# Kernel optimization log

Measured on AMD Instinct MI355X. Metric: run time of the kernel, lower is better.

Reference implementation:

```python
import jax, jax.numpy as jnp
import numpy as np
import math

B, S, E, H = 4, 4096, 2048, 16
Dh = E // H  # 128


def setup_inputs() -> dict:
    key = jax.random.key(0)
    ks = jax.random.split(key, 8)
    s = 1.0 / math.sqrt(E)
    return {
        "x": jax.random.normal(ks[0], (B, S, E), dtype=jnp.float32),
        "Wz": jax.random.uniform(ks[1], (E, E), jnp.float32, -s, s),
        "bz": jax.random.uniform(ks[2], (E,), jnp.float32, -s, s),
        "Wx": jax.random.uniform(ks[3], (E, E), jnp.float32, -s, s),
        "bx": jax.random.uniform(ks[4], (E,), jnp.float32, -s, s),
        "phase": jax.random.normal(ks[5], (H, Dh), dtype=jnp.float32),
        "Wo": jax.random.uniform(ks[6], (E, E), jnp.float32, -s, s),
        "bo": jax.random.uniform(ks[7], (E,), jnp.float32, -s, s),
    }


def reference(x, Wz, bz, Wx, bx, phase, Wo, bo):
    # torch nn.Linear: y = x @ W.T + b  (W stored [out, in])
    z = x @ Wz.T + bz                     # [B,S,E]
    xs = x @ Wx.T + bx                    # [B,S,E]
    z_h = z.reshape(B, S, H, Dh)
    x_h = xs.reshape(B, S, H, Dh)
    # elementwise phase modulation of query heads
    mod = z_h * jnp.sin(phase)            # [B,S,H,Dh] * [H,Dh]
    # NOTE: heads are on axis -2 (no transpose to [B,H,S,Dh]),
    # so scores contract over Dh giving per-token HEAD-mixing: [B,S,H,H]
    scores = jnp.einsum('bshd,bsgd->bshg', mod, x_h) / math.sqrt(Dh)
    w = jax.nn.softmax(scores, axis=-1)   # softmax over head axis g
    att = jnp.einsum('bshg,bsgd->bshd', w, x_h)  # [B,S,H,Dh]
    att = att.reshape(B, S, E)
    return att @ Wo.T + bo
```

## Files before the change

### kernel.cpp

```cpp
#include <hip/hip_runtime.h>
#include <hip/hip_bf16.h>

#define TOK 16384
#define E 2048
#define DH 128

using bf16x8 = __attribute__((ext_vector_type(8))) __bf16;
using f32x4  = __attribute__((ext_vector_type(4))) float;
using u16x8  = __attribute__((ext_vector_type(8))) unsigned short;

static __device__ __forceinline__ unsigned short f2bf(float f) {
  union { float f; unsigned u; } x; x.f = f;
  unsigned r = x.u + 0x7fffu + ((x.u >> 16) & 1u);
  return (unsigned short)(r >> 16);
}

static __device__ __forceinline__ void gload_lds16(const unsigned short* g, unsigned short* l) {
  __builtin_amdgcn_global_load_lds(
      (const __attribute__((address_space(1))) void*)g,
      (__attribute__((address_space(3))) void*)l, 16, 0, 0);
}

static __device__ __forceinline__ void cvt8(const float* __restrict__ src,
                                            unsigned short* __restrict__ dst,
                                            float sc) {
  const float4* p = reinterpret_cast<const float4*>(src);
  float4 v0 = p[0], v1 = p[1];
  u16x8 o;
  o[0] = f2bf(v0.x * sc); o[1] = f2bf(v0.y * sc); o[2] = f2bf(v0.z * sc); o[3] = f2bf(v0.w * sc);
  o[4] = f2bf(v1.x * sc); o[5] = f2bf(v1.y * sc); o[6] = f2bf(v1.z * sc); o[7] = f2bf(v1.w * sc);
  *reinterpret_cast<u16x8*>(dst) = o;
}

__global__ __launch_bounds__(256) void prep_all(const float* __restrict__ x,
                                                const float* __restrict__ Wz,
                                                const float* __restrict__ Wx,
                                                const float* __restrict__ Wo,
                                                const float* __restrict__ bz,
                                                const float* __restrict__ bx,
                                                const float* __restrict__ phase,
                                                unsigned short* __restrict__ x_bf,
                                                unsigned short* __restrict__ wzx,
                                                unsigned short* __restrict__ wo_bf,
                                                float* __restrict__ bzx) {
  const int N0 = TOK * E / 8;
  const int N1 = E * E / 8;
  const int NB = (2 * E) / 8;
  const float rs = 0.08838834764831845f;
  const int total = N0 + 3 * N1 + NB;
  const int stride = gridDim.x * blockDim.x;
  for (int i = blockIdx.x * blockDim.x + threadIdx.x; i < total; i += stride) {
    if (i < N0) {
      cvt8(x + (size_t)i * 8, x_bf + (size_t)i * 8, 1.0f);
    } else if (i < N0 + N1) {
      const int j = i - N0;
      const float sc = sinf(phase[j >> 8]) * rs;
      cvt8(Wz + (size_t)j * 8, wzx + (size_t)j * 8, sc);
    } else if (i < N0 + 2 * N1) {
      const int j = i - N0 - N1;
      cvt8(Wx + (size_t)j * 8, wzx + (size_t)E * E + (size_t)j * 8, 1.0f);
    } else if (i < N0 + 3 * N1) {
      const int j = i - N0 - 2 * N1;
      cvt8(Wo + (size_t)j * 8, wo_bf + (size_t)j * 8, 1.0f);
    } else {
      const int j = i - N0 - 3 * N1;
#pragma unroll
      for (int k = 0; k < 8; ++k) {
        const int idx = j * 8 + k;
        bzx[idx] = (idx < E) ? bz[idx] * sinf(phase[idx]) * rs : bx[idx - E];
      }
    }
  }
}

#define MFMA16 __builtin_amdgcn_mfma_f32_16x16x32_bf16

static __device__ __forceinline__ bf16x8 ldf(const unsigned short* buf, int row, int slot) {
  return *reinterpret_cast<const bf16x8*>(buf + row * 64 + ((slot ^ (row & 7)) << 3));
}

static __device__ __forceinline__ void stage_half(const unsigned short* gbase, int ld,
                                                  unsigned short* dsthalf,
                                                  int r, int slot, int wave) {
#pragma unroll
  for (int c = 0; c < 2; ++c)
    gload_lds16(gbase + (size_t)(c * 64 + r) * ld + slot * 8,
                dsthalf + c * 4096 + wave * 512);
}

static __device__ __forceinline__ void quad(f32x4 (&acc)[8][4], const bf16x8 (&a)[4][2],
                                            const bf16x8 (&b)[2][2], int mh, int nh) {
#pragma unroll
  for (int mi = 0; mi < 4; ++mi)
#pragma unroll
    for (int ni = 0; ni < 2; ++ni)
#pragma unroll
      for (int kk = 0; kk < 2; ++kk)
        acc[mh * 4 + mi][nh * 2 + ni] =
            MFMA16(a[mi][kk], b[ni][kk], acc[mh * 4 + mi][nh * 2 + ni], 0, 0, 0);
}

#define PH_BAR()  __builtin_amdgcn_s_barrier()
#define VMCNT(n)  asm volatile("s_waitcnt vmcnt(" #n ")" ::: "memory")
#define PRIO1()   __builtin_amdgcn_s_setprio(1)
#define PRIO0()   __builtin_amdgcn_s_setprio(0)

#define LD_A(dst, buf, base)                                             \
  _Pragma("unroll")                                                      \
  for (int mi = 0; mi < 4; ++mi)                                         \
    _Pragma("unroll")                                                    \
    for (int kk = 0; kk < 2; ++kk)                                       \
      dst[mi][kk] = ldf(buf, (base) + mi * 16, kk * 4 + grp);

#define LD_B(dst, buf, base)                                             \
  _Pragma("unroll")                                                      \
  for (int ni = 0; ni < 2; ++ni)                                         \
    _Pragma("unroll")                                                    \
    for (int kk = 0; kk < 2; ++kk)                                       \
      dst[ni][kk] = ldf(buf, (base) + ni * 16, kk * 4 + grp);

template <bool LAST>
static __device__ __forceinline__ void k_iter(
    const unsigned short* __restrict__ Ag, const unsigned short* __restrict__ Bg,
    int K_, int lda, int t,
    unsigned short* sA0, unsigned short* sA1, unsigned short* sB0, unsigned short* sB1,
    int r, int slot, int wave, int grp, int rA, int rB,
    bf16x8 (&bP)[2][2], bf16x8 (&bQ)[2][2], f32x4 (&acc)[8][4]) {
  const size_t k1 = (size_t)(t + 1) * 64, k2 = (size_t)(t + 2) * 64, k3 = (size_t)(t + 3) * 64;
  const size_t hA = (size_t)128 * lda, hB = (size_t)128 * K_;
  bf16x8 aF[4][2], b1F[2][2];

  LD_A(aF, sA0, rA);
  stage_half(Ag + k1, lda, sA1, r, slot, wave);
  PRIO1(); quad(acc, aF, bP, 0, 0); PRIO0();
  LD_B(b1F, sB0, rB + 32);
  stage_half(Ag + hA + k1, lda, sA1 + 8192, r, slot, wave);
  PRIO1(); quad(acc, aF, b1F, 0, 1); PRIO0();
  VMCNT(4);
  PH_BAR();

  LD_A(aF, sA0, rA + 64);
  if (!LAST) stage_half(Bg + k2, K_, sB0, r, slot, wave);
  PRIO1(); quad(acc, aF, b1F, 1, 1); PRIO0();
  LD_B(bQ, sB1, rB);
  if (!LAST) stage_half(Bg + hB + k2, K_, sB0 + 8192, r, slot, wave);
  PRIO1(); quad(acc, aF, bP, 1, 0); PRIO0();
  if (!LAST) { VMCNT(4); } else { VMCNT(0); }
  PH_BAR();

  LD_A(aF, sA1, rA);
  if (!LAST) stage_half(Ag + k2, lda, sA0, r, slot, wave);
  PRIO1(); quad(acc, aF, bQ, 0, 0); PRIO0();
  LD_B(b1F, sB1, rB + 32);
  if (!LAST) stage_half(Ag + hA + k2, lda, sA0 + 8192, r, slot, wave);
  PRIO1(); quad(acc, aF, b1F, 0, 1); PRIO0();
  if (!LAST) { VMCNT(4); }
  PH_BAR();

  LD_A(aF, sA1, rA + 64);
  if (!LAST) stage_half(Bg + k3, K_, sB1, r, slot, wave);
  PRIO1(); quad(acc, aF, b1F, 1, 1); PRIO0();
  if (!LAST) {
    LD_B(bP, sB0, rB);
    stage_half(Bg + hB + k3, K_, sB1 + 8192, r, slot, wave);
  }
  PRIO1(); quad(acc, aF, bQ, 1, 0); PRIO0();
  if (!LAST) { VMCNT(4); }
  PH_BAR();
}

template <bool OUT_BF16>
__global__ __launch_bounds__(512, 2) void gemm256(const unsigned short* __restrict__ A,
                                                  const unsigned short* __restrict__ Bm,
                                                  const float* __restrict__ bias,
                                                  void* __restrict__ C,
                                                  int M, int N, int K_, int lda) {
  extern __shared__ unsigned short lds[];
  unsigned short* sA0 = lds;
  unsigned short* sA1 = lds + 16384;
  unsigned short* sB0 = lds + 32768;
  unsigned short* sB1 = lds + 49152;

  const int nbn = N >> 8;
  const int bid = blockIdx.x;
  const int swz = (bid & 7) * ((int)gridDim.x >> 3) + (bid >> 3);
  const int by = swz / nbn, bx = swz % nbn;
  const int tm = by << 8, tn = bx << 8;

  const int tid = threadIdx.x;
  const int wave = tid >> 6, lane = tid & 63;
  const int g16 = lane & 15, grp = lane >> 4;
  const int wm = wave >> 2, wn = wave & 3;
  const int rA = wm * 128 + g16;
  const int rB = wn * 64 + g16;
  const int r = tid >> 3;
  const int slot = (tid & 7) ^ ((tid >> 3) & 7);

  const unsigned short* Ag = A + (size_t)tm * lda;
  const unsigned short* Bg = Bm + (size_t)tn * K_;
  const size_t hA = (size_t)128 * lda, hB = (size_t)128 * K_;

  f32x4 acc[8][4];
#pragma unroll
  for (int i = 0; i < 8; ++i)
#pragma unroll
    for (int j = 0; j < 4; ++j) acc[i][j] = (f32x4){0.f, 0.f, 0.f, 0.f};

  bf16x8 bP[2][2], bQ[2][2];

  stage_half(Ag, lda, sA0, r, slot, wave);
  stage_half(Ag + hA, lda, sA0 + 8192, r, slot, wave);
  stage_half(Bg, K_, sB0, r, slot, wave);
  stage_half(Bg + hB, K_, sB0 + 8192, r, slot, wave);
  stage_half(Bg + 64, K_, sB1, r, slot, wave);
  stage_half(Bg + hB + 64, K_, sB1 + 8192, r, slot, wave);
  VMCNT(4);
  __builtin_amdgcn_s_barrier();
  LD_B(bP, sB0, rB);

  const int NI = K_ >> 7;
#pragma unroll 1
  for (int i = 0; i < NI - 1; ++i)
    k_iter<false>(Ag, Bg, K_, lda, 2 * i, sA0, sA1, sB0, sB1, r, slot, wave, grp, rA, rB,
                  bP, bQ, acc);
  k_iter<true>(Ag, Bg, K_, lda, 2 * (NI - 1), sA0, sA1, sB0, sB1, r, slot, wave, grp, rA, rB,
               bP, bQ, acc);

#pragma unroll
  for (int mi = 0; mi < 8; ++mi) {
#pragma unroll
    for (int ni = 0; ni < 4; ++ni) {
      const int row = tm + wm * 128 + mi * 16 + grp * 4;
      const int col = tn + wn * 64 + ni * 16 + g16;
      const float bv = bias[col];
#pragma unroll
      for (int j = 0; j < 4; ++j) {
        const float v = acc[mi][ni][j] + bv;
        if (OUT_BF16)
          ((unsigned short*)C)[(size_t)(row + j) * N + col] = f2bf(v);
        else
          ((float*)C)[(size_t)(row + j) * N + col] = v;
      }
    }
  }
}

__global__ __launch_bounds__(512) void attn_kernel(const unsigned short* __restrict__ zc,
                                                   unsigned short* __restrict__ attq) {
  __shared__ __align__(16) unsigned short xs_lds[8][16][136];
  __shared__ float w_lds[8][16][17];

  const int wave = threadIdx.x >> 6, lane = threadIdx.x & 63;
  const int token = (blockIdx.x << 3) | wave;
  const unsigned short* modp = zc + (size_t)token * (2 * E);
  const unsigned short* xsp  = modp + E;
  const int g16 = lane & 15, grp = lane >> 4;

  bf16x8 a[4], b[4];
#pragma unroll
  for (int kk = 0; kk < 4; ++kk) {
    a[kk] = *reinterpret_cast<const bf16x8*>(modp + g16 * DH + kk * 32 + grp * 8);
    b[kk] = *reinterpret_cast<const bf16x8*>(xsp  + g16 * DH + kk * 32 + grp * 8);
  }
#pragma unroll
  for (int kk = 0; kk < 4; ++kk)
    *reinterpret_cast<bf16x8*>(&xs_lds[wave][g16][kk * 32 + grp * 8]) = b[kk];

  f32x4 sc = (f32x4){0.f, 0.f, 0.f, 0.f};
#pragma unroll
  for (int kk = 0; kk < 4; ++kk)
    sc = MFMA16(a[kk], b[kk], sc, 0, 0, 0);

  float w4[4];
#pragma unroll
  for (int j = 0; j < 4; ++j) {
    float s = sc[j];
    float m = s;
#pragma unroll
    for (int off = 1; off < 16; off <<= 1) m = fmaxf(m, __shfl_xor(m, off));
    float e = __expf(s - m);
    float t = e;
#pragma unroll
    for (int off = 1; off < 16; off <<= 1) t += __shfl_xor(t, off);
    w4[j] = e / t;
  }
#pragma unroll
  for (int j = 0; j < 4; ++j) w_lds[wave][grp * 4 + j][g16] = w4[j];

  __syncthreads();

  float acc[32];
#pragma unroll
  for (int i = 0; i < 32; ++i) acc[i] = 0.f;
#pragma unroll
  for (int g = 0; g < 16; ++g) {
    const float wg = w_lds[wave][g16][g];
#pragma unroll
    for (int c = 0; c < 4; ++c) {
      bf16x8 xv = *reinterpret_cast<const bf16x8*>(&xs_lds[wave][g][grp * 32 + c * 8]);
#pragma unroll
      for (int j = 0; j < 8; ++j) acc[c * 8 + j] += wg * (float)xv[j];
    }
  }

  unsigned short* op = attq + (size_t)token * E + g16 * DH + grp * 32;
#pragma unroll
  for (int c = 0; c < 4; ++c) {
    u16x8 o;
#pragma unroll
    for (int j = 0; j < 8; ++j) o[j] = f2bf(acc[c * 8 + j]);
    *reinterpret_cast<u16x8*>(op + c * 8) = o;
  }
}

extern "C" void kernel_launch(void* const* d_in, const int* in_sizes, int n_in,
                              void* d_out, int out_size, void* d_ws, size_t ws_size,
                              hipStream_t stream) {
  const float* x     = (const float*)d_in[0];
  const float* Wz    = (const float*)d_in[1];
  const float* bz    = (const float*)d_in[2];
  const float* Wx    = (const float*)d_in[3];
  const float* bx    = (const float*)d_in[4];
  const float* phase = (const float*)d_in[5];
  const float* Wo    = (const float*)d_in[6];
  const float* bo    = (const float*)d_in[7];

  char* p = (char*)d_ws;
  unsigned short* x_bf  = (unsigned short*)p; p += (size_t)TOK * E * 2;
  unsigned short* C12   = (unsigned short*)p; p += (size_t)TOK * 2 * E * 2;
  unsigned short* wzx   = (unsigned short*)p; p += (size_t)2 * E * E * 2;
  unsigned short* wo_bf = (unsigned short*)p; p += (size_t)E * E * 2;
  float* bzx            = (float*)p;          p += (size_t)2 * E * 4;

  hipFuncSetAttribute((const void*)gemm256<true>,
                      hipFuncAttributeMaxDynamicSharedMemorySize, 131072);
  hipFuncSetAttribute((const void*)gemm256<false>,
                      hipFuncAttributeMaxDynamicSharedMemorySize, 131072);

  prep_all<<<2048, 256, 0, stream>>>(x, Wz, Wx, Wo, bz, bx, phase, x_bf, wzx, wo_bf, bzx);

  gemm256<true><<<dim3((TOK / 256) * (2 * E / 256)), 512, 131072, stream>>>(
      x_bf, wzx, bzx, C12, TOK, 2 * E, E, E);
  attn_kernel<<<TOK / 8, 512, 0, stream>>>(C12, x_bf);
  gemm256<false><<<dim3((TOK / 256) * (E / 256)), 512, 131072, stream>>>(
      x_bf, wo_bf, bo, (float*)d_out, TOK, E, E, E);
}
```

Baseline: 454.6 us.

## Restructure GEMM main loop to triple-buffered B with one barrier per k-tile

Replaces the two-tile unrolled four-phase k_iter schedule with a simple per-k-tile loop. A stays double-buffered and B becomes triple-buffered, with buffer pointers rotated each iteration and a single wait plus barrier per tile. B is prefetched two tiles ahead. The aim is fewer barriers and a deeper B prefetch. In exchange, dynamic LDS per block rises from 128 KB to 160 KB, which fills the CU's LDS, and fragment loads are interleaved less finely with the MFMA work.

```diff
diff --git a/kernel.cpp b/kernel.cpp
--- a/kernel.cpp
+++ b/kernel.cpp
@@ -119,56 +119,6 @@
     for (int kk = 0; kk < 2; ++kk)                                       \
       dst[ni][kk] = ldf(buf, (base) + ni * 16, kk * 4 + grp);
 
-template <bool LAST>
-static __device__ __forceinline__ void k_iter(
-    const unsigned short* __restrict__ Ag, const unsigned short* __restrict__ Bg,
-    int K_, int lda, int t,
-    unsigned short* sA0, unsigned short* sA1, unsigned short* sB0, unsigned short* sB1,
-    int r, int slot, int wave, int grp, int rA, int rB,
-    bf16x8 (&bP)[2][2], bf16x8 (&bQ)[2][2], f32x4 (&acc)[8][4]) {
-  const size_t k1 = (size_t)(t + 1) * 64, k2 = (size_t)(t + 2) * 64, k3 = (size_t)(t + 3) * 64;
-  const size_t hA = (size_t)128 * lda, hB = (size_t)128 * K_;
-  bf16x8 aF[4][2], b1F[2][2];
-
-  LD_A(aF, sA0, rA);
-  stage_half(Ag + k1, lda, sA1, r, slot, wave);
-  PRIO1(); quad(acc, aF, bP, 0, 0); PRIO0();
-  LD_B(b1F, sB0, rB + 32);
-  stage_half(Ag + hA + k1, lda, sA1 + 8192, r, slot, wave);
-  PRIO1(); quad(acc, aF, b1F, 0, 1); PRIO0();
-  VMCNT(4);
-  PH_BAR();
-
-  LD_A(aF, sA0, rA + 64);
-  if (!LAST) stage_half(Bg + k2, K_, sB0, r, slot, wave);
-  PRIO1(); quad(acc, aF, b1F, 1, 1); PRIO0();
-  LD_B(bQ, sB1, rB);
-  if (!LAST) stage_half(Bg + hB + k2, K_, sB0 + 8192, r, slot, wave);
-  PRIO1(); quad(acc, aF, bP, 1, 0); PRIO0();
-  if (!LAST) { VMCNT(4); } else { VMCNT(0); }
-  PH_BAR();
-
-  LD_A(aF, sA1, rA);
-  if (!LAST) stage_half(Ag + k2, lda, sA0, r, slot, wave);
-  PRIO1(); quad(acc, aF, bQ, 0, 0); PRIO0();
-  LD_B(b1F, sB1, rB + 32);
-  if (!LAST) stage_half(Ag + hA + k2, lda, sA0 + 8192, r, slot, wave);
-  PRIO1(); quad(acc, aF, b1F, 0, 1); PRIO0();
-  if (!LAST) { VMCNT(4); }
-  PH_BAR();
-
-  LD_A(aF, sA1, rA + 64);
-  if (!LAST) stage_half(Bg + k3, K_, sB1, r, slot, wave);
-  PRIO1(); quad(acc, aF, b1F, 1, 1); PRIO0();
-  if (!LAST) {
-    LD_B(bP, sB0, rB);
-    stage_half(Bg + hB + k3, K_, sB1 + 8192, r, slot, wave);
-  }
-  PRIO1(); quad(acc, aF, bQ, 1, 0); PRIO0();
-  if (!LAST) { VMCNT(4); }
-  PH_BAR();
-}
-
 template <bool OUT_BF16>
 __global__ __launch_bounds__(512, 2) void gemm256(const unsigned short* __restrict__ A,
                                                   const unsigned short* __restrict__ Bm,
@@ -176,10 +126,6 @@
                                                   void* __restrict__ C,
                                                   int M, int N, int K_, int lda) {
   extern __shared__ unsigned short lds[];
-  unsigned short* sA0 = lds;
-  unsigned short* sA1 = lds + 16384;
-  unsigned short* sB0 = lds + 32768;
-  unsigned short* sB1 = lds + 49152;
 
   const int nbn = N >> 8;
   const int bid = blockIdx.x;
@@ -206,25 +152,52 @@
 #pragma unroll
     for (int j = 0; j < 4; ++j) acc[i][j] = (f32x4){0.f, 0.f, 0.f, 0.f};
 
-  bf16x8 bP[2][2], bQ[2][2];
-
-  stage_half(Ag, lda, sA0, r, slot, wave);
-  stage_half(Ag + hA, lda, sA0 + 8192, r, slot, wave);
-  stage_half(Bg, K_, sB0, r, slot, wave);
-  stage_half(Bg + hB, K_, sB0 + 8192, r, slot, wave);
-  stage_half(Bg + 64, K_, sB1, r, slot, wave);
-  stage_half(Bg + hB + 64, K_, sB1 + 8192, r, slot, wave);
+  unsigned short* pa0 = lds;
+  unsigned short* pa1 = lds + 16384;
+  unsigned short* pb0 = lds + 32768;
+  unsigned short* pb1 = lds + 49152;
+  unsigned short* pb2 = lds + 65536;
+
+  stage_half(Ag, lda, pa0, r, slot, wave);
+  stage_half(Ag + hA, lda, pa0 + 8192, r, slot, wave);
+  stage_half(Bg, K_, pb0, r, slot, wave);
+  stage_half(Bg + hB, K_, pb0 + 8192, r, slot, wave);
+  stage_half(Bg + 64, K_, pb1, r, slot, wave);
+  stage_half(Bg + hB + 64, K_, pb1 + 8192, r, slot, wave);
   VMCNT(4);
   __builtin_amdgcn_s_barrier();
-  LD_B(bP, sB0, rB);
-
-  const int NI = K_ >> 7;
+
+  const int NT = K_ >> 6;
 #pragma unroll 1
-  for (int i = 0; i < NI - 1; ++i)
-    k_iter<false>(Ag, Bg, K_, lda, 2 * i, sA0, sA1, sB0, sB1, r, slot, wave, grp, rA, rB,
-                  bP, bQ, acc);
-  k_iter<true>(Ag, Bg, K_, lda, 2 * (NI - 1), sA0, sA1, sB0, sB1, r, slot, wave, grp, rA, rB,
-               bP, bQ, acc);
+  for (int t = 0; t < NT; ++t) {
+    bf16x8 aF[4][2], b0F[2][2], b1F[2][2];
+
+    LD_A(aF, pa0, rA);
+    LD_B(b0F, pb0, rB);
+    if (t + 1 < NT) {
+      const size_t k1 = (size_t)(t + 1) * 64;
+      stage_half(Ag + k1, lda, pa1, r, slot, wave);
+      stage_half(Ag + hA + k1, lda, pa1 + 8192, r, slot, wave);
+    }
+    PRIO1(); quad(acc, aF, b0F, 0, 0); PRIO0();
+
+    LD_B(b1F, pb0, rB + 32);
+    if (t + 2 < NT) {
+      const size_t k2 = (size_t)(t + 2) * 64;
+      stage_half(Bg + k2, K_, pb2, r, slot, wave);
+      stage_half(Bg + hB + k2, K_, pb2 + 8192, r, slot, wave);
+    }
+    PRIO1(); quad(acc, aF, b1F, 0, 1); PRIO0();
+
+    LD_A(aF, pa0, rA + 64);
+    PRIO1(); quad(acc, aF, b1F, 1, 1); PRIO0();
+    PRIO1(); quad(acc, aF, b0F, 1, 0); PRIO0();
+
+    if (t + 2 < NT)      { VMCNT(4); PH_BAR(); }
+    else if (t + 1 < NT) { VMCNT(0); PH_BAR(); }
+    unsigned short* tA = pa0; pa0 = pa1; pa1 = tA;
+    unsigned short* tB = pb0; pb0 = pb1; pb1 = pb2; pb2 = tB;
+  }
 
 #pragma unroll
   for (int mi = 0; mi < 8; ++mi) {
@@ -333,15 +306,15 @@
   float* bzx            = (float*)p;          p += (size_t)2 * E * 4;
 
   hipFuncSetAttribute((const void*)gemm256<true>,
-                      hipFuncAttributeMaxDynamicSharedMemorySize, 131072);
+                      hipFuncAttributeMaxDynamicSharedMemorySize, 163840);
   hipFuncSetAttribute((const void*)gemm256<false>,
-                      hipFuncAttributeMaxDynamicSharedMemorySize, 131072);
+                      hipFuncAttributeMaxDynamicSharedMemorySize, 163840);
 
   prep_all<<<2048, 256, 0, stream>>>(x, Wz, Wx, Wo, bz, bx, phase, x_bf, wzx, wo_bf, bzx);
 
-  gemm256<true><<<dim3((TOK / 256) * (2 * E / 256)), 512, 131072, stream>>>(
+  gemm256<true><<<dim3((TOK / 256) * (2 * E / 256)), 512, 163840, stream>>>(
       x_bf, wzx, bzx, C12, TOK, 2 * E, E, E);
   attn_kernel<<<TOK / 8, 512, 0, stream>>>(C12, x_bf);
-  gemm256<false><<<dim3((TOK / 256) * (E / 256)), 512, 131072, stream>>>(
+  gemm256<false><<<dim3((TOK / 256) * (E / 256)), 512, 163840, stream>>>(
       x_bf, wo_bf, bo, (float*)d_out, TOK, E, E, E);
 }
```

Measured after the change: 459.3 us. No clear change (+1.0%).
